# Optimization experiments

Measured on AMD Instinct MI355X. Metric: run time of the kernel, lower is better.

The kernel has to match this reference:

```python
import jax, jax.numpy as jnp
import numpy as np

N_NODES = 50000
ITER_PROPAGATE = 1


def setup_inputs() -> dict:
    key = jax.random.key(0)
    ks = jax.random.split(key, 14)
    N, D, A, L, E = 50000, 128, 64, 4, 400000
    s = 1.0 / np.sqrt(D)
    return {
        "h": jax.random.normal(ks[0], (N, D), dtype=jnp.float32),
        "x": jax.random.normal(ks[1], (N, A), dtype=jnp.float32),
        "edges_src": jax.random.randint(ks[2], (L, E), 0, N, dtype=jnp.int32),
        "edges_dst": jax.random.randint(ks[3], (L, E), 0, N, dtype=jnp.int32),
        "W_act": jax.random.normal(ks[4], (L, D, D), dtype=jnp.float32) * s,
        "b_act": jnp.zeros((1, D), dtype=jnp.float32),
        "GRU_W_z": jax.random.normal(ks[5], (D, D), dtype=jnp.float32) * s,
        "GRU_W_r": jax.random.normal(ks[6], (D, D), dtype=jnp.float32) * s,
        "GRU_W": jax.random.normal(ks[7], (D, D), dtype=jnp.float32) * s,
        "GRU_U_z": jax.random.normal(ks[8], (D, D), dtype=jnp.float32) * s,
        "GRU_U_r": jax.random.normal(ks[9], (D, D), dtype=jnp.float32) * s,
        "GRU_U": jax.random.normal(ks[10], (D, D), dtype=jnp.float32) * s,
        "rep_kernel": jax.random.normal(ks[11], (D + A, D), dtype=jnp.float32) * (1.0 / np.sqrt(D + A)),
        "rep_bias": jnp.zeros((1, D), dtype=jnp.float32),
    }


def _activate(h, edges_src, edges_dst, W_act, b_act):
    # per-label gather of source states, per-label dense matmul, scatter-add to dst
    D = h.shape[-1]
    msgs = jnp.einsum("led,ldf->lef", h[edges_src], W_act)  # [L, E, D]
    a = jax.ops.segment_sum(msgs.reshape(-1, D), edges_dst.reshape(-1),
                            num_segments=N_NODES)  # [N, D]
    return a + b_act


def reference(h, x, edges_src, edges_dst, W_act, b_act,
              GRU_W_z, GRU_W_r, GRU_W, GRU_U_z, GRU_U_r, GRU_U,
              rep_kernel, rep_bias):
    for _ in range(ITER_PROPAGATE):
        a = _activate(h, edges_src, edges_dst, W_act, b_act)
        z = jax.nn.sigmoid(a @ GRU_W_z + h @ GRU_U_z)
        r = jax.nn.sigmoid(a @ GRU_W_r + h @ GRU_U_r)
        h_hat = jnp.tanh(a @ GRU_W + (r * h) @ GRU_U)
        h = (1.0 - z) * h + z * h_hat
    return jnp.concatenate([h, x], axis=-1) @ rep_kernel + rep_bias
```

## Files before the change

kernel.cpp:

```cpp
#include <hip/hip_runtime.h>

#define NND 50000
#define DIM 128
#define ADIM 64
#define NLBL 4
#define NEDGE 400000
#define NB (NLBL*NND)
#define LE (NLBL*NEDGE)
#define SCAN_NBLK 196
#define NSLICE 8
#define SLICEW 6250
#define NCHUNK 256
#define CPE (LE/NCHUNK)

typedef _Float16 f16;
typedef _Float16 f16x2 __attribute__((ext_vector_type(2)));
typedef _Float16 f16x8 __attribute__((ext_vector_type(8)));
typedef float f32x4 __attribute__((ext_vector_type(4)));

__device__ __forceinline__ float sigmoid_(float x){ return 1.f/(1.f+__expf(-x)); }
__device__ __forceinline__ float tanh_(float x){ return 1.f - 2.f/(__expf(2.f*x)+1.f); }

__global__ void prep_kernel(const float* __restrict__ h, const float* __restrict__ x,
    const float* __restrict__ Wact,
    const float* __restrict__ Wz, const float* __restrict__ Wr, const float* __restrict__ Ww,
    const float* __restrict__ Uz, const float* __restrict__ Ur, const float* __restrict__ Uu,
    const float* __restrict__ rep,
    f16* __restrict__ hh, f16* __restrict__ xh,
    f16* __restrict__ wcat, f16* __restrict__ wzr, f16* __restrict__ wh, f16* __restrict__ wrep)
{
  const int TOT = NND*DIM + NND*ADIM + 65536 + 65536 + 32768 + 24576;
  for (int i = blockIdx.x*blockDim.x + threadIdx.x; i < TOT; i += gridDim.x*blockDim.x) {
    int j = i;
    if (j < NND*DIM) { hh[j] = (f16)h[j]; continue; }
    j -= NND*DIM;
    if (j < NND*ADIM) { xh[j] = (f16)x[j]; continue; }
    j -= NND*ADIM;
    if (j < 65536) {
      int f = j >> 9, k = j & 511; int l = k >> 7, d = k & 127;
      wcat[j] = (f16)Wact[l*16384 + d*128 + f]; continue;
    }
    j -= 65536;
    if (j < 65536) {
      int r = j >> 8, k = j & 255; float v;
      if (r < 128) v = (k < 128) ? Wz[k*128 + r] : Uz[(k-128)*128 + r];
      else { int rr = r-128; v = (k < 128) ? Wr[k*128 + rr] : Ur[(k-128)*128 + rr]; }
      wzr[j] = (f16)v; continue;
    }
    j -= 65536;
    if (j < 32768) {
      int r = j >> 8, k = j & 255;
      wh[j] = (f16)((k < 128) ? Ww[k*128 + r] : Uu[(k-128)*128 + r]); continue;
    }
    j -= 32768;
    { int r = j / 192, k = j - r*192;
      wrep[j] = (f16)rep[k*128 + r]; }
  }
}

__global__ void hist_kernel(const int* __restrict__ dst, int* __restrict__ cnt) {
  const int slice = blockIdx.x & (NSLICE-1);
  const int chunk = blockIdx.x >> 3;
  const int lo = slice * SLICEW, hi = lo + SLICEW;
  const int base = chunk * CPE, end = base + CPE;
  for (int i = base + threadIdx.x; i < end; i += blockDim.x) {
    int d = dst[i];
    if (d >= lo && d < hi) {
      int l = i / NEDGE;
      atomicAdd(&cnt[l*NND + d], 1);
    }
  }
}

__global__ void scan_reduce_kernel(const int* __restrict__ cnt, int* __restrict__ bsum) {
  __shared__ int s[256];
  int t = threadIdx.x; int base = blockIdx.x*1024;
  int v = 0;
  for (int i = t; i < 1024; i += 256) { int idx = base + i; if (idx < NB) v += cnt[idx]; }
  s[t] = v; __syncthreads();
  for (int o = 128; o > 0; o >>= 1) { if (t < o) s[t] += s[t+o]; __syncthreads(); }
  if (t == 0) bsum[blockIdx.x] = s[0];
}

__global__ void scan_top_kernel(int* __restrict__ bsum) {
  __shared__ int s[256];
  int t = threadIdx.x;
  int v = (t < SCAN_NBLK) ? bsum[t] : 0;
  s[t] = v; __syncthreads();
  for (int o = 1; o < 256; o <<= 1) { int u = (t >= o) ? s[t-o] : 0; __syncthreads(); s[t] += u; __syncthreads(); }
  if (t < SCAN_NBLK) bsum[t] = s[t] - v;
}

__global__ void scan_final_kernel(const int* __restrict__ cnt, const int* __restrict__ bsum,
                                  int* __restrict__ off, int* __restrict__ cur) {
  __shared__ int s[256];
  int t = threadIdx.x; int base = blockIdx.x*1024 + t*4;
  int c0=0,c1=0,c2=0,c3=0;
  if (base+0 < NB) c0 = cnt[base+0];
  if (base+1 < NB) c1 = cnt[base+1];
  if (base+2 < NB) c2 = cnt[base+2];
  if (base+3 < NB) c3 = cnt[base+3];
  int tot = c0+c1+c2+c3;
  s[t] = tot; __syncthreads();
  for (int o = 1; o < 256; o <<= 1) { int u = (t >= o) ? s[t-o] : 0; __syncthreads(); s[t] += u; __syncthreads(); }
  int pre = bsum[blockIdx.x] + s[t] - tot;
  if (base+0 < NB) { off[base+0]=pre; cur[base+0]=pre; } pre += c0;
  if (base+1 < NB) { off[base+1]=pre; cur[base+1]=pre; } pre += c1;
  if (base+2 < NB) { off[base+2]=pre; cur[base+2]=pre; } pre += c2;
  if (base+3 < NB) { off[base+3]=pre; cur[base+3]=pre; }
}

__global__ void fill_kernel(const int* __restrict__ src, const int* __restrict__ dst,
                            int* __restrict__ cur, int* __restrict__ csr) {
  const int slice = blockIdx.x & (NSLICE-1);
  const int chunk = blockIdx.x >> 3;
  const int lo = slice * SLICEW, hi = lo + SLICEW;
  const int base = chunk * CPE, end = base + CPE;
  for (int i = base + threadIdx.x; i < end; i += blockDim.x) {
    int d = dst[i];
    if (d >= lo && d < hi) {
      int l = i / NEDGE;
      int pos = atomicAdd(&cur[l*NND + d], 1);
      csr[pos] = src[i];
    }
  }
}

__global__ __launch_bounds__(256) void agg_kernel(const f16* __restrict__ hh,
    const int* __restrict__ csr, const int* __restrict__ off, const int* __restrict__ cnt,
    f16* __restrict__ g)
{
  int n = blockIdx.x;
  int l = threadIdx.x >> 6;
  int lane = threadIdx.x & 63;
  int b = l*NND + n;
  int beg = off[b], c = cnt[b];
  const f16* hp = hh + lane*2;
  float ax = 0.f, ay = 0.f;
  for (int base = 0; base < c; base += 64) {
    int m = c - base; if (m > 64) m = 64;
    int my = 0;
    if (lane < m) my = csr[beg + base + lane];
    int j = 0;
    for (; j + 4 <= m; j += 4) {
      int s0 = __shfl(my, j), s1 = __shfl(my, j+1), s2 = __shfl(my, j+2), s3 = __shfl(my, j+3);
      f16x2 v0 = *(const f16x2*)(hp + (size_t)s0*DIM);
      f16x2 v1 = *(const f16x2*)(hp + (size_t)s1*DIM);
      f16x2 v2 = *(const f16x2*)(hp + (size_t)s2*DIM);
      f16x2 v3 = *(const f16x2*)(hp + (size_t)s3*DIM);
      ax += (float)v0.x + (float)v1.x + (float)v2.x + (float)v3.x;
      ay += (float)v0.y + (float)v1.y + (float)v2.y + (float)v3.y;
    }
    for (; j < m; ++j) {
      int s0 = __shfl(my, j);
      f16x2 v0 = *(const f16x2*)(hp + (size_t)s0*DIM);
      ax += (float)v0.x; ay += (float)v0.y;
    }
  }
  f16x2 o2; o2.x = (f16)ax; o2.y = (f16)ay;
  *(f16x2*)(g + (size_t)n*512 + l*128 + lane*2) = o2;
}

__global__ __launch_bounds__(256, 2) void mega_kernel(
    const f16* __restrict__ g, const f16* __restrict__ hh, const f16* __restrict__ xh,
    const f16* __restrict__ wcat, const f16* __restrict__ wzr, const f16* __restrict__ whw,
    const f16* __restrict__ wrep, const float* __restrict__ bact, const float* __restrict__ rbias,
    float* __restrict__ out, int M)
{
  __shared__ __align__(16) char smem[65536];
  char* h_t = smem;
  char* a_t = smem + 16384;
  char* z_t = smem + 32768;
  char* w_t = smem + 49152;
  const int tid = threadIdx.x;
  const int w = tid >> 6, lane = tid & 63;
  const int lr = lane >> 4, lc = lane & 15;
  const int r0 = blockIdx.x * 64;

  auto swz = [](int r, int c) { return r*256 + (((c ^ r) & 7) | (c & 8))*16; };

#pragma unroll
  for (int it = 0; it < 4; ++it) {
    int idx = it*256 + tid;
    int r = idx >> 4, c = idx & 15;
    int gr = r0 + r;
    uint4 vh = make_uint4(0u,0u,0u,0u);
    if (gr < M) vh = *(const uint4*)(hh + (size_t)gr*128 + c*8);
    *(uint4*)(h_t + swz(r, c)) = vh;
  }

  {
    f32x4 acc[4][2];
#pragma unroll
    for (int i = 0; i < 4; ++i) { acc[i][0] = (f32x4){0,0,0,0}; acc[i][1] = (f32x4){0,0,0,0}; }
#pragma unroll
    for (int ks = 0; ks < 16; ++ks) {
      f16x8 af[4], bf[2];
#pragma unroll
      for (int fm = 0; fm < 4; ++fm) {
        int gr = r0 + fm*16 + lc;
        uint4 u = make_uint4(0u,0u,0u,0u);
        if (gr < M) u = *(const uint4*)(g + (size_t)gr*512 + ks*32 + lr*8);
        af[fm] = *reinterpret_cast<const f16x8*>(&u);
      }
#pragma unroll
      for (int fn = 0; fn < 2; ++fn)
        bf[fn] = *(const f16x8*)(wcat + (size_t)(w*32 + fn*16 + lc)*512 + ks*32 + lr*8);
#pragma unroll
      for (int fm = 0; fm < 4; ++fm)
#pragma unroll
        for (int fn = 0; fn < 2; ++fn)
          acc[fm][fn] = __builtin_amdgcn_mfma_f32_16x16x32_f16(af[fm], bf[fn], acc[fm][fn], 0, 0, 0);
    }
#pragma unroll
    for (int fm = 0; fm < 4; ++fm)
#pragma unroll
      for (int fn = 0; fn < 2; ++fn) {
        int col = w*32 + fn*16 + lc;
#pragma unroll
        for (int t = 0; t < 4; ++t) {
          int row = fm*16 + lr*4 + t;
          float v = acc[fm][fn][t] + bact[col];
          *(f16*)(a_t + swz(row, col >> 3) + (col & 7)*2) = (f16)v;
        }
      }
  }
  __syncthreads();

  {
    const int qc0 = w*64;
    f32x4 acc[4][4];
#pragma unroll
    for (int i = 0; i < 4; ++i)
#pragma unroll
      for (int j = 0; j < 4; ++j) acc[i][j] = (f32x4){0,0,0,0};
#pragma unroll
    for (int ks = 0; ks < 8; ++ks) {
      const char* asrc = (ks < 4) ? a_t : h_t;
      int cb = (ks & 3)*4 + lr;
      f16x8 af[4], bf[4];
#pragma unroll
      for (int fm = 0; fm < 4; ++fm)
        af[fm] = *(const f16x8*)(asrc + swz(fm*16 + lc, cb));
#pragma unroll
      for (int fn = 0; fn < 4; ++fn)
        bf[fn] = *(const f16x8*)(wzr + (size_t)(qc0 + fn*16 + lc)*256 + ks*32 + lr*8);
#pragma unroll
      for (int fm = 0; fm < 4; ++fm)
#pragma unroll
        for (int fn = 0; fn < 4; ++fn)
          acc[fm][fn] = __builtin_amdgcn_mfma_f32_16x16x32_f16(af[fm], bf[fn], acc[fm][fn], 0, 0, 0);
    }
#pragma unroll
    for (int fm = 0; fm < 4; ++fm)
#pragma unroll
      for (int fn = 0; fn < 4; ++fn) {
        int col = qc0 + fn*16 + lc;
#pragma unroll
        for (int t = 0; t < 4; ++t) {
          int row = fm*16 + lr*4 + t;
          float sg = sigmoid_(acc[fm][fn][t]);
          if (qc0 < 128) {
            *(f16*)(z_t + swz(row, col >> 3) + (col & 7)*2) = (f16)sg;
          } else {
            int c2 = col - 128;
            float h0 = (float)*(const f16*)(h_t + swz(row, c2 >> 3) + (c2 & 7)*2);
            *(f16*)(w_t + swz(row, c2 >> 3) + (c2 & 7)*2) = (f16)(sg * h0);
          }
        }
      }
  }
  __syncthreads();

  {
    const int qc0 = w*32;
    f32x4 acc[4][2];
#pragma unroll
    for (int i = 0; i < 4; ++i) { acc[i][0] = (f32x4){0,0,0,0}; acc[i][1] = (f32x4){0,0,0,0}; }
#pragma unroll
    for (int ks = 0; ks < 8; ++ks) {
      const char* asrc = (ks < 4) ? a_t : w_t;
      int cb = (ks & 3)*4 + lr;
      f16x8 af[4], bf[2];
#pragma unroll
      for (int fm = 0; fm < 4; ++fm)
        af[fm] = *(const f16x8*)(asrc + swz(fm*16 + lc, cb));
#pragma unroll
      for (int fn = 0; fn < 2; ++fn)
        bf[fn] = *(const f16x8*)(whw + (size_t)(qc0 + fn*16 + lc)*256 + ks*32 + lr*8);
#pragma unroll
      for (int fm = 0; fm < 4; ++fm)
#pragma unroll
        for (int fn = 0; fn < 2; ++fn)
          acc[fm][fn] = __builtin_amdgcn_mfma_f32_16x16x32_f16(af[fm], bf[fn], acc[fm][fn], 0, 0, 0);
    }
    __syncthreads();
#pragma unroll
    for (int fm = 0; fm < 4; ++fm)
#pragma unroll
      for (int fn = 0; fn < 2; ++fn) {
        int col = qc0 + fn*16 + lc;
#pragma unroll
        for (int t = 0; t < 4; ++t) {
          int row = fm*16 + lr*4 + t;
          float th = tanh_(acc[fm][fn][t]);
          float zz = (float)*(const f16*)(z_t + swz(row, col >> 3) + (col & 7)*2);
          float h0 = (float)*(const f16*)(h_t + swz(row, col >> 3) + (col & 7)*2);
          *(f16*)(w_t + swz(row, col >> 3) + (col & 7)*2) = (f16)((1.f - zz)*h0 + zz*th);
        }
      }
  }
  __syncthreads();

  {
    const int qc0 = w*32;
    f32x4 acc[4][2];
#pragma unroll
    for (int i = 0; i < 4; ++i) { acc[i][0] = (f32x4){0,0,0,0}; acc[i][1] = (f32x4){0,0,0,0}; }
#pragma unroll
    for (int ks = 0; ks < 6; ++ks) {
      f16x8 af[4], bf[2];
      if (ks < 4) {
#pragma unroll
        for (int fm = 0; fm < 4; ++fm)
          af[fm] = *(const f16x8*)(w_t + swz(fm*16 + lc, ks*4 + lr));
      } else {
#pragma unroll
        for (int fm = 0; fm < 4; ++fm) {
          int gr = r0 + fm*16 + lc;
          uint4 u = make_uint4(0u,0u,0u,0u);
          if (gr < M) u = *(const uint4*)(xh + (size_t)gr*64 + (ks - 4)*32 + lr*8);
          af[fm] = *reinterpret_cast<const f16x8*>(&u);
        }
      }
#pragma unroll
      for (int fn = 0; fn < 2; ++fn)
        bf[fn] = *(const f16x8*)(wrep + (size_t)(qc0 + fn*16 + lc)*192 + ks*32 + lr*8);
#pragma unroll
      for (int fm = 0; fm < 4; ++fm)
#pragma unroll
        for (int fn = 0; fn < 2; ++fn)
          acc[fm][fn] = __builtin_amdgcn_mfma_f32_16x16x32_f16(af[fm], bf[fn], acc[fm][fn], 0, 0, 0);
    }
#pragma unroll
    for (int fm = 0; fm < 4; ++fm)
#pragma unroll
      for (int fn = 0; fn < 2; ++fn) {
        int col = qc0 + fn*16 + lc;
#pragma unroll
        for (int t = 0; t < 4; ++t) {
          int row = fm*16 + lr*4 + t;
          int grow = r0 + row;
          if (grow < M) out[(size_t)grow*128 + col] = acc[fm][fn][t] + rbias[col];
        }
      }
  }
}

extern "C" void kernel_launch(void* const* d_in, const int* in_sizes, int n_in,
                              void* d_out, int out_size, void* d_ws, size_t ws_size,
                              hipStream_t stream) {
  const float* h    = (const float*)d_in[0];
  const float* x    = (const float*)d_in[1];
  const int*   esrc = (const int*)d_in[2];
  const int*   edst = (const int*)d_in[3];
  const float* Wact = (const float*)d_in[4];
  const float* bact = (const float*)d_in[5];
  const float* Wz   = (const float*)d_in[6];
  const float* Wr   = (const float*)d_in[7];
  const float* Ww   = (const float*)d_in[8];
  const float* Uz   = (const float*)d_in[9];
  const float* Ur   = (const float*)d_in[10];
  const float* Uu   = (const float*)d_in[11];
  const float* rep  = (const float*)d_in[12];
  const float* rbias= (const float*)d_in[13];
  float* out = (float*)d_out;

  char* ws = (char*)d_ws;
  size_t o = 0;
  auto alloc = [&](size_t bytes) { char* p = ws + o; o += (bytes + 255) & ~(size_t)255; return p; };
  f16* hh   = (f16*)alloc((size_t)NND*DIM*2);
  f16* xh   = (f16*)alloc((size_t)NND*ADIM*2);
  f16* wcat = (f16*)alloc(65536*2);
  f16* wzr  = (f16*)alloc(65536*2);
  f16* whw  = (f16*)alloc(32768*2);
  f16* wrep = (f16*)alloc(24576*2);
  int* cnt  = (int*)alloc((size_t)NB*4);
  int* off  = (int*)alloc((size_t)NB*4);
  int* cur  = (int*)alloc((size_t)NB*4);
  int* bsum = (int*)alloc(SCAN_NBLK*4);
  int* csr  = (int*)alloc((size_t)LE*4);
  f16* g    = (f16*)alloc((size_t)NND*512*2);

  hipMemsetAsync(cnt, 0, (size_t)NB*4, stream);
  prep_kernel<<<2048, 256, 0, stream>>>(h, x, Wact, Wz, Wr, Ww, Uz, Ur, Uu, rep,
                                        hh, xh, wcat, wzr, whw, wrep);
  hist_kernel<<<NCHUNK*NSLICE, 256, 0, stream>>>(edst, cnt);
  scan_reduce_kernel<<<SCAN_NBLK, 256, 0, stream>>>(cnt, bsum);
  scan_top_kernel<<<1, 256, 0, stream>>>(bsum);
  scan_final_kernel<<<SCAN_NBLK, 256, 0, stream>>>(cnt, bsum, off, cur);
  fill_kernel<<<NCHUNK*NSLICE, 256, 0, stream>>>(esrc, edst, cur, csr);
  agg_kernel<<<NND, 256, 0, stream>>>(hh, csr, off, cnt, g);

  const int GB = (NND + 63) / 64;
  mega_kernel<<<GB, 256, 0, stream>>>(g, hh, xh, wcat, wzr, whw, wrep, bact, rbias, out, NND);
}
```

Measured before the change: 439.5 us.

## Split aggregation GEMM into LDS-tiled kernel and slim GRU kernel for occupancy

The first GEMM (g[N,512] x wcat) moves out of the fused kernel into a dedicated 128x128-tile kernel that stages A and B through swizzled LDS with register double-buffering, and it writes the activation a to global memory in fp16. The remaining GRU and readout kernel halves its shared memory to 32KB and raises launch bounds to 4 blocks per CU. It reads a and h from global instead of LDS and recomputes r*h and the GRU blend on the fly inside the MFMA operand loads. This trades an extra 12.8MB round-trip and a second launch for better reuse of g and weights and higher occupancy.

```diff
diff --git a/kernel.cpp b/kernel.cpp
--- a/kernel.cpp
+++ b/kernel.cpp
@@ -161,71 +161,115 @@
   *(f16x2*)(g + (size_t)n*512 + l*128 + lane*2) = o2;
 }
 
-__global__ __launch_bounds__(256, 2) void mega_kernel(
-    const f16* __restrict__ g, const f16* __restrict__ hh, const f16* __restrict__ xh,
-    const f16* __restrict__ wcat, const f16* __restrict__ wzr, const f16* __restrict__ whw,
-    const f16* __restrict__ wrep, const float* __restrict__ bact, const float* __restrict__ rbias,
-    float* __restrict__ out, int M)
+__global__ __launch_bounds__(256, 2) void gemm_a_kernel(
+    const f16* __restrict__ A0, const f16* __restrict__ Wt, const float* __restrict__ bias,
+    f16* __restrict__ O0, int M)
 {
-  __shared__ __align__(16) char smem[65536];
-  char* h_t = smem;
-  char* a_t = smem + 16384;
-  char* z_t = smem + 32768;
-  char* w_t = smem + 49152;
+  constexpr int KT = 512;
+  constexpr int NK = KT / 64;
+  __shared__ __align__(16) char smem[32768];
+  const int tid = threadIdx.x;
+  const int w = tid >> 6, lane = tid & 63;
+  const int wm = w >> 1, wn = w & 1;
+  const int lr = lane >> 4, lc = lane & 15;
+  const int bm0 = blockIdx.x * 128;
+  const int tr = tid >> 3;
+  const int tc = tid & 7;
+
+  f32x4 acc[4][4];
+#pragma unroll
+  for (int i = 0; i < 4; ++i)
+#pragma unroll
+    for (int j = 0; j < 4; ++j) acc[i][j] = (f32x4){0.f,0.f,0.f,0.f};
+
+  auto loadAB = [&](int kt, uint4* a, uint4* b) {
+    const int k0 = kt*64;
+#pragma unroll
+    for (int p = 0; p < 4; ++p) {
+      int rl = p*32 + tr; int gr = bm0 + rl;
+      if (gr < M) a[p] = *(const uint4*)(A0 + (size_t)gr*KT + k0 + tc*8);
+      else a[p] = make_uint4(0u,0u,0u,0u);
+    }
+#pragma unroll
+    for (int p = 0; p < 4; ++p) {
+      int cl = p*32 + tr;
+      b[p] = *(const uint4*)(Wt + (size_t)cl*KT + k0 + tc*8);
+    }
+  };
+
+  uint4 av[4], bv[4];
+  loadAB(0, av, bv);
+#pragma unroll
+  for (int kt = 0; kt < NK; ++kt) {
+    __syncthreads();
+#pragma unroll
+    for (int p = 0; p < 4; ++p) {
+      int rl = p*32 + tr;
+      int sw = (tc ^ (tr & 7)) * 16;
+      *(uint4*)(smem + rl*128 + sw) = av[p];
+      *(uint4*)(smem + 16384 + rl*128 + sw) = bv[p];
+    }
+    uint4 a2[4], b2[4];
+    bool more = (kt+1 < NK);
+    if (more) loadAB(kt+1, a2, b2);
+    __syncthreads();
+#pragma unroll
+    for (int kk = 0; kk < 2; ++kk) {
+      f16x8 af[4], bf[4];
+      const int cb = ((kk*4 + lr) ^ (lc & 7)) * 16;
+#pragma unroll
+      for (int fm = 0; fm < 4; ++fm)
+        af[fm] = *(const f16x8*)(smem + (wm*64 + fm*16 + lc)*128 + cb);
+#pragma unroll
+      for (int fn = 0; fn < 4; ++fn)
+        bf[fn] = *(const f16x8*)(smem + 16384 + (wn*64 + fn*16 + lc)*128 + cb);
+#pragma unroll
+      for (int fm = 0; fm < 4; ++fm)
+#pragma unroll
+        for (int fn = 0; fn < 4; ++fn)
+          acc[fm][fn] = __builtin_amdgcn_mfma_f32_16x16x32_f16(af[fm], bf[fn], acc[fm][fn], 0, 0, 0);
+    }
+    if (more) {
+#pragma unroll
+      for (int p = 0; p < 4; ++p) { av[p] = a2[p]; bv[p] = b2[p]; }
+    }
+  }
+
+#pragma unroll
+  for (int fm = 0; fm < 4; ++fm) {
+#pragma unroll
+    for (int fn = 0; fn < 4; ++fn) {
+      f32x4 v = acc[fm][fn];
+      int col = wn*64 + fn*16 + lc;
+#pragma unroll
+      for (int t = 0; t < 4; ++t) {
+        int row = bm0 + wm*64 + fm*16 + lr*4 + t;
+        if (row >= M) continue;
+        O0[(size_t)row*128 + col] = (f16)(v[t] + bias[col]);
+      }
+    }
+  }
+}
+
+__global__ __launch_bounds__(256, 4) void mega2_kernel(
+    const f16* __restrict__ ah, const f16* __restrict__ hh, const f16* __restrict__ xh,
+    const f16* __restrict__ wzr, const f16* __restrict__ whw, const f16* __restrict__ wrep,
+    const float* __restrict__ rbias, float* __restrict__ out, int M)
+{
+  __shared__ __align__(16) char smem[32768];
+  char* z_t = smem;
+  char* w_t = smem + 16384;
   const int tid = threadIdx.x;
   const int w = tid >> 6, lane = tid & 63;
   const int lr = lane >> 4, lc = lane & 15;
   const int r0 = blockIdx.x * 64;
 
   auto swz = [](int r, int c) { return r*256 + (((c ^ r) & 7) | (c & 8))*16; };
-
-#pragma unroll
-  for (int it = 0; it < 4; ++it) {
-    int idx = it*256 + tid;
-    int r = idx >> 4, c = idx & 15;
-    int gr = r0 + r;
-    uint4 vh = make_uint4(0u,0u,0u,0u);
-    if (gr < M) vh = *(const uint4*)(hh + (size_t)gr*128 + c*8);
-    *(uint4*)(h_t + swz(r, c)) = vh;
-  }
-
-  {
-    f32x4 acc[4][2];
-#pragma unroll
-    for (int i = 0; i < 4; ++i) { acc[i][0] = (f32x4){0,0,0,0}; acc[i][1] = (f32x4){0,0,0,0}; }
-#pragma unroll
-    for (int ks = 0; ks < 16; ++ks) {
-      f16x8 af[4], bf[2];
-#pragma unroll
-      for (int fm = 0; fm < 4; ++fm) {
-        int gr = r0 + fm*16 + lc;
-        uint4 u = make_uint4(0u,0u,0u,0u);
-        if (gr < M) u = *(const uint4*)(g + (size_t)gr*512 + ks*32 + lr*8);
-        af[fm] = *reinterpret_cast<const f16x8*>(&u);
-      }
-#pragma unroll
-      for (int fn = 0; fn < 2; ++fn)
-        bf[fn] = *(const f16x8*)(wcat + (size_t)(w*32 + fn*16 + lc)*512 + ks*32 + lr*8);
-#pragma unroll
-      for (int fm = 0; fm < 4; ++fm)
-#pragma unroll
-        for (int fn = 0; fn < 2; ++fn)
-          acc[fm][fn] = __builtin_amdgcn_mfma_f32_16x16x32_f16(af[fm], bf[fn], acc[fm][fn], 0, 0, 0);
-    }
-#pragma unroll
-    for (int fm = 0; fm < 4; ++fm)
-#pragma unroll
-      for (int fn = 0; fn < 2; ++fn) {
-        int col = w*32 + fn*16 + lc;
-#pragma unroll
-        for (int t = 0; t < 4; ++t) {
-          int row = fm*16 + lr*4 + t;
-          float v = acc[fm][fn][t] + bact[col];
-          *(f16*)(a_t + swz(row, col >> 3) + (col & 7)*2) = (f16)v;
-        }
-      }
-  }
-  __syncthreads();
+  auto gldA = [&](const f16* s, int row, int kc) -> f16x8 {
+    uint4 u = make_uint4(0u,0u,0u,0u);
+    if (row < M) u = *(const uint4*)(s + (size_t)row*128 + kc);
+    return *reinterpret_cast<const f16x8*>(&u);
+  };
 
   {
     const int qc0 = w*64;
@@ -236,12 +280,12 @@
       for (int j = 0; j < 4; ++j) acc[i][j] = (f32x4){0,0,0,0};
 #pragma unroll
     for (int ks = 0; ks < 8; ++ks) {
-      const char* asrc = (ks < 4) ? a_t : h_t;
-      int cb = (ks & 3)*4 + lr;
+      const f16* asrc = (ks < 4) ? ah : hh;
+      const int kc = (ks & 3)*32 + lr*8;
       f16x8 af[4], bf[4];
 #pragma unroll
       for (int fm = 0; fm < 4; ++fm)
-        af[fm] = *(const f16x8*)(asrc + swz(fm*16 + lc, cb));
+        af[fm] = gldA(asrc, r0 + fm*16 + lc, kc);
 #pragma unroll
       for (int fn = 0; fn < 4; ++fn)
         bf[fn] = *(const f16x8*)(wzr + (size_t)(qc0 + fn*16 + lc)*256 + ks*32 + lr*8);
@@ -260,13 +304,9 @@
         for (int t = 0; t < 4; ++t) {
           int row = fm*16 + lr*4 + t;
           float sg = sigmoid_(acc[fm][fn][t]);
-          if (qc0 < 128) {
-            *(f16*)(z_t + swz(row, col >> 3) + (col & 7)*2) = (f16)sg;
-          } else {
-            int c2 = col - 128;
-            float h0 = (float)*(const f16*)(h_t + swz(row, c2 >> 3) + (c2 & 7)*2);
-            *(f16*)(w_t + swz(row, c2 >> 3) + (c2 & 7)*2) = (f16)(sg * h0);
-          }
+          if (qc0 < 128) *(f16*)(z_t + swz(row, col >> 3) + (col & 7)*2) = (f16)sg;
+          else { int c2 = col - 128;
+                 *(f16*)(w_t + swz(row, c2 >> 3) + (c2 & 7)*2) = (f16)sg; }
         }
       }
   }
@@ -279,12 +319,20 @@
     for (int i = 0; i < 4; ++i) { acc[i][0] = (f32x4){0,0,0,0}; acc[i][1] = (f32x4){0,0,0,0}; }
 #pragma unroll
     for (int ks = 0; ks < 8; ++ks) {
-      const char* asrc = (ks < 4) ? a_t : w_t;
-      int cb = (ks & 3)*4 + lr;
+      const int kc = (ks & 3)*32 + lr*8;
       f16x8 af[4], bf[2];
-#pragma unroll
-      for (int fm = 0; fm < 4; ++fm)
-        af[fm] = *(const f16x8*)(asrc + swz(fm*16 + lc, cb));
+      if (ks < 4) {
+#pragma unroll
+        for (int fm = 0; fm < 4; ++fm)
+          af[fm] = gldA(ah, r0 + fm*16 + lc, kc);
+      } else {
+#pragma unroll
+        for (int fm = 0; fm < 4; ++fm) {
+          f16x8 rf = *(const f16x8*)(w_t + swz(fm*16 + lc, (ks & 3)*4 + lr));
+          f16x8 hf = gldA(hh, r0 + fm*16 + lc, kc);
+          af[fm] = rf * hf;
+        }
+      }
 #pragma unroll
       for (int fn = 0; fn < 2; ++fn)
         bf[fn] = *(const f16x8*)(whw + (size_t)(qc0 + fn*16 + lc)*256 + ks*32 + lr*8);
@@ -303,10 +351,7 @@
 #pragma unroll
         for (int t = 0; t < 4; ++t) {
           int row = fm*16 + lr*4 + t;
-          float th = tanh_(acc[fm][fn][t]);
-          float zz = (float)*(const f16*)(z_t + swz(row, col >> 3) + (col & 7)*2);
-          float h0 = (float)*(const f16*)(h_t + swz(row, col >> 3) + (col & 7)*2);
-          *(f16*)(w_t + swz(row, col >> 3) + (col & 7)*2) = (f16)((1.f - zz)*h0 + zz*th);
+          *(f16*)(w_t + swz(row, col >> 3) + (col & 7)*2) = (f16)tanh_(acc[fm][fn][t]);
         }
       }
   }
@@ -322,8 +367,13 @@
       f16x8 af[4], bf[2];
       if (ks < 4) {
 #pragma unroll
-        for (int fm = 0; fm < 4; ++fm)
-          af[fm] = *(const f16x8*)(w_t + swz(fm*16 + lc, ks*4 + lr));
+        for (int fm = 0; fm < 4; ++fm) {
+          int sc = ks*4 + lr;
+          f16x8 zf = *(const f16x8*)(z_t + swz(fm*16 + lc, sc));
+          f16x8 tf = *(const f16x8*)(w_t + swz(fm*16 + lc, sc));
+          f16x8 hf = gldA(hh, r0 + fm*16 + lc, ks*32 + lr*8);
+          af[fm] = hf + zf*(tf - hf);
+        }
       } else {
 #pragma unroll
         for (int fm = 0; fm < 4; ++fm) {
@@ -391,6 +441,7 @@
   int* bsum = (int*)alloc(SCAN_NBLK*4);
   int* csr  = (int*)alloc((size_t)LE*4);
   f16* g    = (f16*)alloc((size_t)NND*512*2);
+  f16* ah   = (f16*)alloc((size_t)NND*DIM*2);
 
   hipMemsetAsync(cnt, 0, (size_t)NB*4, stream);
   prep_kernel<<<2048, 256, 0, stream>>>(h, x, Wact, Wz, Wr, Ww, Uz, Ur, Uu, rep,
@@ -402,6 +453,8 @@
   fill_kernel<<<NCHUNK*NSLICE, 256, 0, stream>>>(esrc, edst, cur, csr);
   agg_kernel<<<NND, 256, 0, stream>>>(hh, csr, off, cnt, g);
 
+  const int GM = (NND + 127) / 128;
+  gemm_a_kernel<<<GM, 256, 0, stream>>>(g, wcat, bact, ah, NND);
   const int GB = (NND + 63) / 64;
-  mega_kernel<<<GB, 256, 0, stream>>>(g, hh, xh, wcat, wzr, whw, wrep, bact, rbias, out, NND);
-}
+  mega2_kernel<<<GB, 256, 0, stream>>>(ah, hh, xh, wzr, whw, wrep, rbias, out, NND);
+}
```

Measured after the change: 476.3 us. +8.4%, slower.
